# Optimization experiments

Measured on AMD Instinct MI355X. Metric: run time of the kernel, lower is better.

The kernel has to match this reference:

```python
import jax, jax.numpy as jnp
import numpy as np

B, K, N, D, H, DOUT = 16, 8, 196, 768, 3072, 768


def setup_inputs() -> dict:
    key = jax.random.key(0)
    ks = jax.random.split(key, 5)
    scale_w1 = 1.0 / np.sqrt(D)
    scale_w2 = 1.0 / np.sqrt(H)
    return {
        "slots": jax.random.normal(ks[0], (B, K, D), dtype=jnp.float32),
        "pos_embed": jax.random.normal(ks[1], (N, D), dtype=jnp.float32) * 0.02,
        "map_alpha": jax.random.normal(ks[2], (N, DOUT), dtype=jnp.float32) * 0.02,
        "W1": jax.random.normal(ks[3], (D, H), dtype=jnp.float32) * scale_w1,
        "b1": jnp.zeros((H,), dtype=jnp.float32),
        "W2": jax.random.normal(ks[4], (H, DOUT), dtype=jnp.float32) * scale_w2,
        "b2": jnp.zeros((DOUT,), dtype=jnp.float32),
    }


def reference(slots, pos_embed, map_alpha, W1, b1, W2, b2):
    b, k, d = slots.shape
    n = pos_embed.shape[0]
    # broadcast slots over patches and add positional embedding: (B,K,N,D)
    tokens = slots[:, :, None, :] + pos_embed[None, None, :, :]
    # 2-layer MLP with ReLU
    h = jax.nn.relu(jnp.einsum('bknd,dh->bknh', tokens, W1) + b1)
    y_k = jnp.einsum('bknh,ho->bkno', h, W2) + b2  # (B,K,N,DOUT)
    # softmax over K of map_alpha expanded over (B,K); identical across K -> uniform 1/K,
    # computed explicitly for faithfulness to the original module
    m_k = jax.nn.softmax(jnp.broadcast_to(map_alpha[None, None, :, :], (b, k, n, map_alpha.shape[1])), axis=1)
    y = jnp.einsum('bknd,bknd->bnd', y_k, m_k)
    return y
```

## Files before the change

### kernel.cpp

```cpp
#include <hip/hip_runtime.h>
#include <hip/hip_bf16.h>
#include <stdint.h>


typedef __attribute__((ext_vector_type(8))) short bf16x8;
typedef __attribute__((ext_vector_type(4))) float f32x4;

#define AS1 __attribute__((address_space(1)))
#define AS3 __attribute__((address_space(3)))

#define WAIT_VM(N) asm volatile("s_waitcnt vmcnt(" #N ")" ::: "memory")
#define BAR()      asm volatile("s_barrier" ::: "memory")
#define BAR_LDS()  asm volatile("s_waitcnt lgkmcnt(0)\ns_barrier" ::: "memory")

static __device__ __forceinline__ void gld_lds16(const void* g, void* l) {
    __builtin_amdgcn_global_load_lds((const AS1 unsigned int*)g,
                                     (AS3 unsigned int*)l, 16, 0, 0);
}

static __device__ __forceinline__ unsigned short f2bf(float f) {
    union { float f; unsigned int u; } v; v.f = f;
    unsigned int u = v.u;
    return (unsigned short)((u + 0x7fffu + ((u >> 16) & 1u)) >> 16);
}

__global__ void k_prep(const float* __restrict__ W1, unsigned short* __restrict__ W1t,
                       const float* __restrict__ S, const float* __restrict__ P,
                       unsigned short* __restrict__ A1) {
    int idx = blockIdx.x * blockDim.x + threadIdx.x;
    const int C1n = 96 * 3072;
    const int PKn = 96 * 384;
    if (idx < C1n) {
        int r  = idx % 3072;
        int kc = idx / 3072;
        unsigned int po[4];
        #pragma unroll
        for (int j = 0; j < 4; ++j) {
            unsigned short lo = f2bf(W1[(size_t)(kc * 8 + 2 * j) * 3072 + r]);
            unsigned short hi = f2bf(W1[(size_t)(kc * 8 + 2 * j + 1) * 3072 + r]);
            po[j] = (unsigned int)lo | ((unsigned int)hi << 16);
        }
        size_t dst = ((size_t)(r >> 6) * 12 + (kc >> 3)) * 4096
                   + (size_t)((kc & 7) * 64 + (r & 63)) * 8;
        *(uint4*)(W1t + dst) = make_uint4(po[0], po[1], po[2], po[3]);
    } else if (idx < C1n + PKn) {
        int t = idx - C1n;
        int r  = t % 384;
        int kc = t / 384;
        uint4 o = make_uint4(0u, 0u, 0u, 0u);
        if (r < 324) {
            const float* src = (r < 128) ? (S + (size_t)r * 768 + kc * 8)
                                         : (P + (size_t)(r - 128) * 768 + kc * 8);
            float4 a = *(const float4*)(src);
            float4 b = *(const float4*)(src + 4);
            o.x = (unsigned int)f2bf(a.x) | ((unsigned int)f2bf(a.y) << 16);
            o.y = (unsigned int)f2bf(a.z) | ((unsigned int)f2bf(a.w) << 16);
            o.z = (unsigned int)f2bf(b.x) | ((unsigned int)f2bf(b.y) << 16);
            o.w = (unsigned int)f2bf(b.z) | ((unsigned int)f2bf(b.w) << 16);
        }
        size_t dst = ((size_t)(r >> 6) * 12 + (kc >> 3)) * 4096
                   + (size_t)((kc & 7) * 64 + (r & 63)) * 8;
        *(uint4*)(A1 + dst) = o;
    }
}

__launch_bounds__(256)
__global__ void k_gemm1_w2t(const unsigned short* __restrict__ A,
                            const unsigned short* __restrict__ Bt,
                            float* __restrict__ C,
                            const float* __restrict__ W2,
                            unsigned short* __restrict__ W2t) {
    const int tid = threadIdx.x;
    if (blockIdx.x >= 288) {
        int idx = (blockIdx.x - 288) * 256 + tid;
        int r  = idx % 768;
        int kc = idx / 768;
        unsigned int po[4];
        #pragma unroll
        for (int j = 0; j < 4; ++j) {
            unsigned short lo = f2bf(W2[(size_t)(kc * 8 + 2 * j) * 768 + r]);
            unsigned short hi = f2bf(W2[(size_t)(kc * 8 + 2 * j + 1) * 768 + r]);
            po[j] = (unsigned int)lo | ((unsigned int)hi << 16);
        }
        size_t dst = ((size_t)(r >> 6) * 48 + (kc >> 3)) * 4096
                   + (size_t)((kc & 7) * 64 + (r & 63)) * 8;
        *(uint4*)(W2t + dst) = make_uint4(po[0], po[1], po[2], po[3]);
        return;
    }

    __shared__ unsigned short sm[3 * 8192];
    const int lane = tid & 63;
    const int wave = tid >> 6;
    const int wm = wave >> 1, wn = wave & 1;
    const int q = lane >> 4, l16 = lane & 15;

    const int id = blockIdx.x;
    const int j  = id >> 3;
    const int nt = (id & 7) * 6 + j % 6;
    const int rt = j / 6;

    const unsigned short* Ab = A  + (size_t)rt * 12 * 4096;
    const unsigned short* Bb = Bt + (size_t)nt * 12 * 4096;

    f32x4 acc[2][2] = {};
    const int offA = (wm * 32 + l16) * 8;
    const int offB = 4096 + (wn * 32 + l16) * 8;

    auto stage = [&](int i, unsigned short* d) {
        const unsigned short* Ag = Ab + (size_t)i * 4096;
        const unsigned short* Bg = Bb + (size_t)i * 4096;
        gld_lds16(Ag + tid * 8,        d + tid * 8);
        gld_lds16(Ag + 2048 + tid * 8, d + 2048 + tid * 8);
        gld_lds16(Bg + tid * 8,        d + 4096 + tid * 8);
        gld_lds16(Bg + 2048 + tid * 8, d + 6144 + tid * 8);
    };
    auto compute = [&](const unsigned short* buf) {
        #pragma unroll
        for (int ks = 0; ks < 2; ++ks) {
            const int ko = (ks * 4 + q) * 512;
            bf16x8 af0 = *(const bf16x8*)(buf + ko + offA);
            bf16x8 af1 = *(const bf16x8*)(buf + ko + offA + 128);
            bf16x8 bf0 = *(const bf16x8*)(buf + ko + offB);
            bf16x8 bf1 = *(const bf16x8*)(buf + ko + offB + 128);
            acc[0][0] = __builtin_amdgcn_mfma_f32_16x16x32_bf16(af0, bf0, acc[0][0], 0, 0, 0);
            acc[0][1] = __builtin_amdgcn_mfma_f32_16x16x32_bf16(af0, bf1, acc[0][1], 0, 0, 0);
            acc[1][0] = __builtin_amdgcn_mfma_f32_16x16x32_bf16(af1, bf0, acc[1][0], 0, 0, 0);
            acc[1][1] = __builtin_amdgcn_mfma_f32_16x16x32_bf16(af1, bf1, acc[1][1], 0, 0, 0);
        }
    };

    unsigned short* s0 = sm;
    unsigned short* s1 = sm + 8192;
    unsigned short* s2 = sm + 16384;

    stage(0, s0);
    stage(1, s1);
    for (int i = 0; i < 12; i += 3) {
        stage(i + 2, s2); WAIT_VM(8);
        BAR(); compute(s0); BAR_LDS();
        if (i + 3 < 12) { stage(i + 3, s0); WAIT_VM(8); } else { WAIT_VM(4); }
        BAR(); compute(s1); BAR_LDS();
        if (i + 4 < 12) { stage(i + 4, s1); WAIT_VM(8); }
        else if (i + 3 < 12) { WAIT_VM(4); }
        else { WAIT_VM(0); }
        BAR(); compute(s2);
        if (i + 3 < 12) BAR_LDS();
    }

    const int row0 = rt * 64 + wm * 32;
    const int col0 = nt * 64 + wn * 32;
    #pragma unroll
    for (int ii = 0; ii < 2; ++ii) {
        #pragma unroll
        for (int jj = 0; jj < 2; ++jj) {
            int col = col0 + jj * 16 + l16;
            #pragma unroll
            for (int r = 0; r < 4; ++r) {
                int row = row0 + ii * 16 + q * 4 + r;
                if (row < 324) C[(size_t)row * 3072 + col] = acc[ii][jj][r];
            }
        }
    }
}

__global__ void k_hbar(const float* __restrict__ C1, const float* __restrict__ b1,
                       unsigned short* __restrict__ Hb) {
    const int bid  = blockIdx.x;
    const int tid  = threadIdx.x;
    const int bx   = bid % 49;
    const int yq   = bid / 49;
    const int lane = tid & 63;
    const int wv   = tid >> 6;
    const int hc   = yq * 4 + wv;
    const int h0   = hc * 8;
    const int bn   = bx * 64 + lane;
    const int b    = bn / 196;
    const int n    = bn - b * 196;
    const float* prow = C1 + (size_t)(128 + n) * 3072 + h0;
    float4 pA = *(const float4*)(prow);
    float4 pB = *(const float4*)(prow + 4);
    float4 bA = *(const float4*)(b1 + h0);
    float4 bB = *(const float4*)(b1 + h0 + 4);
    float pb[8] = { pA.x + bA.x, pA.y + bA.y, pA.z + bA.z, pA.w + bA.w,
                    pB.x + bB.x, pB.y + bB.y, pB.z + bB.z, pB.w + bB.w };
    float acc[8] = {};
    #pragma unroll
    for (int k = 0; k < 8; ++k) {
        const float* srow = C1 + (size_t)(b * 8 + k) * 3072 + h0;
        float4 sA_ = *(const float4*)(srow);
        float4 sB_ = *(const float4*)(srow + 4);
        acc[0] += fmaxf(sA_.x + pb[0], 0.f);
        acc[1] += fmaxf(sA_.y + pb[1], 0.f);
        acc[2] += fmaxf(sA_.z + pb[2], 0.f);
        acc[3] += fmaxf(sA_.w + pb[3], 0.f);
        acc[4] += fmaxf(sB_.x + pb[4], 0.f);
        acc[5] += fmaxf(sB_.y + pb[5], 0.f);
        acc[6] += fmaxf(sB_.z + pb[6], 0.f);
        acc[7] += fmaxf(sB_.w + pb[7], 0.f);
    }
    unsigned int w0 = (unsigned int)f2bf(acc[0] * 0.125f) | ((unsigned int)f2bf(acc[1] * 0.125f) << 16);
    unsigned int w1 = (unsigned int)f2bf(acc[2] * 0.125f) | ((unsigned int)f2bf(acc[3] * 0.125f) << 16);
    unsigned int w2 = (unsigned int)f2bf(acc[4] * 0.125f) | ((unsigned int)f2bf(acc[5] * 0.125f) << 16);
    unsigned int w3 = (unsigned int)f2bf(acc[6] * 0.125f) | ((unsigned int)f2bf(acc[7] * 0.125f) << 16);
    size_t dst = ((size_t)bx * 48 + (hc >> 3)) * 4096
               + (size_t)((hc & 7) * 64 + lane) * 8;
    *(uint4*)(Hb + dst) = make_uint4(w0, w1, w2, w3);
}

__launch_bounds__(512)
__global__ void k_gemm2(const unsigned short* __restrict__ Hb,
                        const unsigned short* __restrict__ W2t,
                        const float* __restrict__ b2, float* __restrict__ out) {
    __shared__ unsigned short sm[3 * 8192];

    const int tid  = threadIdx.x;
    const int lane = tid & 63;
    const int wave = tid >> 6;
    const int kg = wave >> 2;
    const int w  = wave & 3;
    const int wm = w >> 1, wn = w & 1;
    const int q = lane >> 4, l16 = lane & 15;

    const int id = blockIdx.x;
    int rt, nt;
    if (id < 576) { rt = (id & 7) + 8 * ((id >> 3) % 6); nt = (id >> 3) / 6; }
    else          { rt = 48; nt = id - 576; }

    const unsigned short* Ab = Hb  + (size_t)rt * 48 * 4096;
    const unsigned short* Bb = W2t + (size_t)nt * 48 * 4096;

    f32x4 acc[2][2] = {};

    auto stage = [&](int i, unsigned short* d) {
        gld_lds16(Ab + (size_t)i * 4096 + tid * 8, d + tid * 8);
        gld_lds16(Bb + (size_t)i * 4096 + tid * 8, d + 4096 + tid * 8);
    };

    const int offA = (wm * 32 + l16) * 8;
    const int offB = 4096 + (wn * 32 + l16) * 8;
    const int ko   = (kg * 4 + q) * 512;
    auto compute = [&](const unsigned short* buf) {
        bf16x8 af0 = *(const bf16x8*)(buf + ko + offA);
        bf16x8 af1 = *(const bf16x8*)(buf + ko + offA + 128);
        bf16x8 bf0 = *(const bf16x8*)(buf + ko + offB);
        bf16x8 bf1 = *(const bf16x8*)(buf + ko + offB + 128);
        acc[0][0] = __builtin_amdgcn_mfma_f32_16x16x32_bf16(af0, bf0, acc[0][0], 0, 0, 0);
        acc[0][1] = __builtin_amdgcn_mfma_f32_16x16x32_bf16(af0, bf1, acc[0][1], 0, 0, 0);
        acc[1][0] = __builtin_amdgcn_mfma_f32_16x16x32_bf16(af1, bf0, acc[1][0], 0, 0, 0);
        acc[1][1] = __builtin_amdgcn_mfma_f32_16x16x32_bf16(af1, bf1, acc[1][1], 0, 0, 0);
    };

    unsigned short* s0 = sm;
    unsigned short* s1 = sm + 8192;
    unsigned short* s2 = sm + 16384;

    stage(0, s0);
    stage(1, s1);
    for (int i = 0; i < 48; i += 3) {
        stage(i + 2, s2); WAIT_VM(4);
        BAR(); compute(s0); BAR_LDS();
        if (i + 3 < 48) { stage(i + 3, s0); WAIT_VM(4); } else { WAIT_VM(2); }
        BAR(); compute(s1); BAR_LDS();
        if (i + 4 < 48) { stage(i + 4, s1); WAIT_VM(4); }
        else if (i + 3 < 48) { WAIT_VM(2); }
        else { WAIT_VM(0); }
        BAR(); compute(s2);
        if (i + 3 < 48) BAR_LDS();
    }

    float* smf = (float*)sm;
    __syncthreads();
    if (kg == 1) {
        #pragma unroll
        for (int ii = 0; ii < 2; ++ii)
            #pragma unroll
            for (int jj = 0; jj < 2; ++jj)
                *(f32x4*)(smf + ((size_t)((w * 4 + ii * 2 + jj) * 64 + lane)) * 4) = acc[ii][jj];
    }
    __syncthreads();
    if (kg == 1) return;
    #pragma unroll
    for (int ii = 0; ii < 2; ++ii)
        #pragma unroll
        for (int jj = 0; jj < 2; ++jj) {
            f32x4 p = *(const f32x4*)(smf + ((size_t)((w * 4 + ii * 2 + jj) * 64 + lane)) * 4);
            acc[ii][jj] += p;
        }

    const int row0 = rt * 64 + wm * 32;
    const int col0 = nt * 64 + wn * 32;
    #pragma unroll
    for (int ii = 0; ii < 2; ++ii) {
        #pragma unroll
        for (int jj = 0; jj < 2; ++jj) {
            int col = col0 + jj * 16 + l16;
            float bv = b2[col];
            #pragma unroll
            for (int r = 0; r < 4; ++r) {
                int row = row0 + ii * 16 + q * 4 + r;
                out[(size_t)row * 768 + col] = acc[ii][jj][r] + bv;
            }
        }
    }
}

extern "C" void kernel_launch(void* const* d_in, const int* in_sizes, int n_in,
                              void* d_out, int out_size, void* d_ws, size_t ws_size,
                              hipStream_t stream) {
    const float* slots  = (const float*)d_in[0];
    const float* pos    = (const float*)d_in[1];
    const float* W1     = (const float*)d_in[3];
    const float* b1     = (const float*)d_in[4];
    const float* W2     = (const float*)d_in[5];
    const float* b2     = (const float*)d_in[6];
    float* out = (float*)d_out;

    size_t off = 0;
    auto alloc = [&](size_t bytes) {
        void* p = (char*)d_ws + off;
        off += (bytes + 255) & ~(size_t)255;
        return p;
    };
    unsigned short* W1t = (unsigned short*)alloc((size_t)3072 * 768 * 2);
    unsigned short* W2t = (unsigned short*)alloc((size_t)768 * 3072 * 2);
    unsigned short* A1  = (unsigned short*)alloc((size_t)384 * 768 * 2);
    float*          C1  = (float*)alloc((size_t)384 * 3072 * 4);
    unsigned short* Hb  = (unsigned short*)alloc((size_t)49 * 48 * 4096 * 2);

    k_prep<<<1296, 256, 0, stream>>>(W1, W1t, slots, pos, A1);
    k_gemm1_w2t<<<1440, 256, 0, stream>>>(A1, W1t, C1, W2, W2t);
    k_hbar<<<4704, 256, 0, stream>>>(C1, b1, Hb);
    k_gemm2<<<588, 512, 0, stream>>>(Hb, W2t, b2, out);
}
```

Measured before the change: 129.0 us.

## Split-K GEMM2 into two halves with reduce kernel; move W2 transpose into prep

The second GEMM now splits its K dimension (3072) into two halves. This doubles the block count from 588 to 1176 so more CUs stay busy, and each half writes fp32 partials to separate buffers. A new reduce kernel sums the two partials and adds b2. The W2 bf16 transpose moves from the GEMM1 launch into the prep kernel, so GEMM1 runs alone with 288 blocks. The cost is an extra kernel launch plus roughly 19 MB of partial writes and reads.

```diff
diff --git a/kernel.cpp b/kernel.cpp
--- a/kernel.cpp
+++ b/kernel.cpp
@@ -26,7 +26,8 @@
 
 __global__ void k_prep(const float* __restrict__ W1, unsigned short* __restrict__ W1t,
                        const float* __restrict__ S, const float* __restrict__ P,
-                       unsigned short* __restrict__ A1) {
+                       unsigned short* __restrict__ A1,
+                       const float* __restrict__ W2, unsigned short* __restrict__ W2t) {
     int idx = blockIdx.x * blockDim.x + threadIdx.x;
     const int C1n = 96 * 3072;
     const int PKn = 96 * 384;
@@ -61,20 +62,10 @@
         size_t dst = ((size_t)(r >> 6) * 12 + (kc >> 3)) * 4096
                    + (size_t)((kc & 7) * 64 + (r & 63)) * 8;
         *(uint4*)(A1 + dst) = o;
-    }
-}
-
-__launch_bounds__(256)
-__global__ void k_gemm1_w2t(const unsigned short* __restrict__ A,
-                            const unsigned short* __restrict__ Bt,
-                            float* __restrict__ C,
-                            const float* __restrict__ W2,
-                            unsigned short* __restrict__ W2t) {
-    const int tid = threadIdx.x;
-    if (blockIdx.x >= 288) {
-        int idx = (blockIdx.x - 288) * 256 + tid;
-        int r  = idx % 768;
-        int kc = idx / 768;
+    } else {
+        int t = idx - C1n - PKn;
+        int r  = t % 768;
+        int kc = t / 768;
         unsigned int po[4];
         #pragma unroll
         for (int j = 0; j < 4; ++j) {
@@ -85,10 +76,15 @@
         size_t dst = ((size_t)(r >> 6) * 48 + (kc >> 3)) * 4096
                    + (size_t)((kc & 7) * 64 + (r & 63)) * 8;
         *(uint4*)(W2t + dst) = make_uint4(po[0], po[1], po[2], po[3]);
-        return;
-    }
-
+    }
+}
+
+__launch_bounds__(256)
+__global__ void k_gemm1(const unsigned short* __restrict__ A,
+                        const unsigned short* __restrict__ Bt,
+                        float* __restrict__ C) {
     __shared__ unsigned short sm[3 * 8192];
+    const int tid = threadIdx.x;
     const int lane = tid & 63;
     const int wave = tid >> 6;
     const int wm = wave >> 1, wn = wave & 1;
@@ -210,7 +206,7 @@
 __launch_bounds__(512)
 __global__ void k_gemm2(const unsigned short* __restrict__ Hb,
                         const unsigned short* __restrict__ W2t,
-                        const float* __restrict__ b2, float* __restrict__ out) {
+                        float* __restrict__ P0, float* __restrict__ P1) {
     __shared__ unsigned short sm[3 * 8192];
 
     const int tid  = threadIdx.x;
@@ -222,12 +218,14 @@
     const int q = lane >> 4, l16 = lane & 15;
 
     const int id = blockIdx.x;
+    const int t  = id >> 1;
+    const int h  = id & 1;
     int rt, nt;
-    if (id < 576) { rt = (id & 7) + 8 * ((id >> 3) % 6); nt = (id >> 3) / 6; }
-    else          { rt = 48; nt = id - 576; }
-
-    const unsigned short* Ab = Hb  + (size_t)rt * 48 * 4096;
-    const unsigned short* Bb = W2t + (size_t)nt * 48 * 4096;
+    if (t < 576) { rt = (t & 7) + 8 * ((t >> 3) % 6); nt = (t >> 3) / 6; }
+    else         { rt = 48; nt = t - 576; }
+
+    const unsigned short* Ab = Hb  + (size_t)rt * 48 * 4096 + (size_t)h * 24 * 4096;
+    const unsigned short* Bb = W2t + (size_t)nt * 48 * 4096 + (size_t)h * 24 * 4096;
 
     f32x4 acc[2][2] = {};
 
@@ -256,16 +254,16 @@
 
     stage(0, s0);
     stage(1, s1);
-    for (int i = 0; i < 48; i += 3) {
+    for (int i = 0; i < 24; i += 3) {
         stage(i + 2, s2); WAIT_VM(4);
         BAR(); compute(s0); BAR_LDS();
-        if (i + 3 < 48) { stage(i + 3, s0); WAIT_VM(4); } else { WAIT_VM(2); }
+        if (i + 3 < 24) { stage(i + 3, s0); WAIT_VM(4); } else { WAIT_VM(2); }
         BAR(); compute(s1); BAR_LDS();
-        if (i + 4 < 48) { stage(i + 4, s1); WAIT_VM(4); }
-        else if (i + 3 < 48) { WAIT_VM(2); }
+        if (i + 4 < 24) { stage(i + 4, s1); WAIT_VM(4); }
+        else if (i + 3 < 24) { WAIT_VM(2); }
         else { WAIT_VM(0); }
         BAR(); compute(s2);
-        if (i + 3 < 48) BAR_LDS();
+        if (i + 3 < 24) BAR_LDS();
     }
 
     float* smf = (float*)sm;
@@ -287,6 +285,7 @@
             acc[ii][jj] += p;
         }
 
+    float* Pd = h ? P1 : P0;
     const int row0 = rt * 64 + wm * 32;
     const int col0 = nt * 64 + wn * 32;
     #pragma unroll
@@ -294,14 +293,27 @@
         #pragma unroll
         for (int jj = 0; jj < 2; ++jj) {
             int col = col0 + jj * 16 + l16;
-            float bv = b2[col];
             #pragma unroll
             for (int r = 0; r < 4; ++r) {
                 int row = row0 + ii * 16 + q * 4 + r;
-                out[(size_t)row * 768 + col] = acc[ii][jj][r] + bv;
+                Pd[(size_t)row * 768 + col] = acc[ii][jj][r];
             }
         }
     }
+}
+
+__global__ void k_reduce(const float* __restrict__ P0, const float* __restrict__ P1,
+                         const float* __restrict__ b2, float* __restrict__ out) {
+    int i = blockIdx.x * blockDim.x + threadIdx.x;
+    float4 a = ((const float4*)P0)[i];
+    float4 b = ((const float4*)P1)[i];
+    float4 c = ((const float4*)b2)[i % 192];
+    float4 r;
+    r.x = a.x + b.x + c.x;
+    r.y = a.y + b.y + c.y;
+    r.z = a.z + b.z + c.z;
+    r.w = a.w + b.w + c.w;
+    ((float4*)out)[i] = r;
 }
 
 extern "C" void kernel_launch(void* const* d_in, const int* in_sizes, int n_in,
@@ -326,9 +338,12 @@
     unsigned short* A1  = (unsigned short*)alloc((size_t)384 * 768 * 2);
     float*          C1  = (float*)alloc((size_t)384 * 3072 * 4);
     unsigned short* Hb  = (unsigned short*)alloc((size_t)49 * 48 * 4096 * 2);
-
-    k_prep<<<1296, 256, 0, stream>>>(W1, W1t, slots, pos, A1);
-    k_gemm1_w2t<<<1440, 256, 0, stream>>>(A1, W1t, C1, W2, W2t);
+    float*          P0  = (float*)alloc((size_t)3136 * 768 * 4);
+    float*          P1  = (float*)alloc((size_t)3136 * 768 * 4);
+
+    k_prep<<<2448, 256, 0, stream>>>(W1, W1t, slots, pos, A1, W2, W2t);
+    k_gemm1<<<288, 256, 0, stream>>>(A1, W1t, C1);
     k_hbar<<<4704, 256, 0, stream>>>(C1, b1, Hb);
-    k_gemm2<<<588, 512, 0, stream>>>(Hb, W2t, b2, out);
-}
+    k_gemm2<<<1176, 512, 0, stream>>>(Hb, W2t, P0, P1);
+    k_reduce<<<2352, 256, 0, stream>>>(P0, P1, b2, out);
+}
```

Result: no change. 130.8 us (+1.4%).
